# Kernel optimization log

Hardware: AMD Instinct MI355X
Metric: run time of the kernel (lower is better)

## Reference

```python
import jax, jax.numpy as jnp
import numpy as np


def gcn_conv(x, W, b, src, dst, edge_weight):
    """GCNConv: out = A_hat @ (x @ W) + b, with A_hat given as an edge list.
    x: [N, F_in], W: [F_in, F_out], src/dst: [E] int, edge_weight: [E]."""
    N = x.shape[0]
    support = x @ W                                   # [N, F_out] dense GEMM
    msgs = support[src] * edge_weight[:, None]        # [E, F_out] gather + scale
    agg = jax.ops.segment_sum(msgs, dst, num_segments=N)  # [N, F_out] scatter-add
    return agg + b


def setup_inputs() -> dict:
    key = jax.random.key(0)
    ks = jax.random.split(key, 8)
    N, E, F_IN, H, D = 100000, 1600000, 256, 128, 64
    feature = jax.random.normal(ks[0], (N, F_IN), dtype=jnp.float32)
    src = jax.random.randint(ks[1], (E,), 0, N)
    dst = jax.random.randint(ks[2], (E,), 0, N)
    edge_weight = jax.random.uniform(ks[3], (E,), dtype=jnp.float32)
    W1 = jax.random.normal(ks[4], (F_IN, H), dtype=jnp.float32) / np.sqrt(F_IN).astype(np.float32)
    b1 = jnp.zeros((H,), jnp.float32)
    W2 = jax.random.normal(ks[5], (H, D), dtype=jnp.float32) / np.sqrt(H).astype(np.float32)
    b2 = jnp.zeros((D,), jnp.float32)
    return {"feature": feature, "src": src, "dst": dst, "edge_weight": edge_weight,
            "W1": W1, "b1": b1, "W2": W2, "b2": b2}


def reference(feature, src, dst, edge_weight, W1, b1, W2, b2):
    # layer 1: GCNConv -> relu (dropout is identity in eval mode)
    x1 = jax.nn.relu(gcn_conv(feature, W1, b1, src, dst, edge_weight))
    # layer 2: GCNConv -> log_softmax over feature dim
    x2 = gcn_conv(x1, W2, b2, src, dst, edge_weight)
    return (x1, jax.nn.log_softmax(x2, axis=1))
```

## Files before the change

kernel.cpp:

```cpp
#include <hip/hip_runtime.h>
#include <hip/hip_bf16.h>
#include <type_traits>


typedef unsigned short u16;
typedef unsigned char  u8;

__device__ __forceinline__ u16 f2bf(float x) {
    union { float f; unsigned u; } v; v.f = x;
    const unsigned r = v.u + 0x7FFFu + ((v.u >> 16) & 1u);
    return (u16)(r >> 16);
}
__device__ __forceinline__ float bf2f(unsigned h) {
    union { unsigned u; float f; } v; v.u = h << 16;
    return v.f;
}
__device__ __forceinline__ float uaf(unsigned u) {
    union { unsigned u; float f; } v; v.u = u;
    return v.f;
}
__device__ __forceinline__ unsigned fau(float f) {
    union { float f; unsigned u; } v; v.f = f;
    return v.u;
}

using short8  = __attribute__((ext_vector_type(8))) short;
using float4v = __attribute__((ext_vector_type(4))) float;

#define TILE_A 8192

template <typename AT, int BNt>
__device__ __forceinline__ void gemm_body(
    const int bix, const AT* __restrict__ A, const u16* __restrict__ BT,
    u16* __restrict__ C, const int M, const int K)
{
    constexpr int BMt = 128;
    constexpr int WAVES_N = BNt / 64;
    constexpr int WROWS = 4 / WAVES_N;
    constexpr int WMF = BMt / (16 * WROWS);
    constexpr int WNF = 4;

    __shared__ __align__(16) u16 As[BMt * 32];
    __shared__ __align__(16) u16 Bs[BNt * 32];

    const int tid  = threadIdx.x;
    const int lane = tid & 63;
    const int w    = tid >> 6;
    const int m0   = bix * BMt;

    const int wm = (w % WROWS) * (WMF * 16);
    const int wn = (w / WROWS) * 64;

    const int fm = lane & 15;
    const int kh = lane >> 4;

    float4v acc[WMF][WNF] = {};

    for (int k0 = 0; k0 < K; k0 += 32) {
        __syncthreads();
        if constexpr (std::is_same<AT, float>::value) {
#pragma unroll
            for (int i = 0; i < 4; ++i) {
                const int s   = i * 256 + tid;
                const int row = s >> 3;
                const int seg = s & 7;
                const int gr  = min(m0 + row, M - 1);
                const float4 v = *(const float4*)&A[(size_t)gr * K + k0 + seg * 4];
                ushort4 o;
                o.x = f2bf(v.x); o.y = f2bf(v.y); o.z = f2bf(v.z); o.w = f2bf(v.w);
                *(ushort4*)&As[row * 32 + seg * 4] = o;
            }
        } else {
#pragma unroll
            for (int i = 0; i < 2; ++i) {
                const int s   = i * 256 + tid;
                const int row = s >> 2;
                const int seg = s & 3;
                const int gr  = min(m0 + row, M - 1);
                *(uint4*)&As[row * 32 + seg * 8] =
                    *(const uint4*)&A[(size_t)gr * K + k0 + seg * 8];
            }
        }
#pragma unroll
        for (int i = 0; i < BNt * 4 / 256; ++i) {
            const int s   = i * 256 + tid;
            const int row = s >> 2;
            const int seg = s & 3;
            *(uint4*)&Bs[row * 32 + seg * 8] =
                *(const uint4*)&BT[(size_t)row * K + k0 + seg * 8];
        }
        __syncthreads();

        short8 af[WMF], bfr[WNF];
#pragma unroll
        for (int i = 0; i < WMF; ++i)
            af[i] = *(const short8*)&As[(wm + i * 16 + fm) * 32 + kh * 8];
#pragma unroll
        for (int j = 0; j < WNF; ++j)
            bfr[j] = *(const short8*)&Bs[(wn + j * 16 + fm) * 32 + kh * 8];
#pragma unroll
        for (int i = 0; i < WMF; ++i)
#pragma unroll
            for (int j = 0; j < WNF; ++j)
                acc[i][j] = __builtin_amdgcn_mfma_f32_16x16x32_bf16(
                    af[i], bfr[j], acc[i][j], 0, 0, 0);
    }

#pragma unroll
    for (int i = 0; i < WMF; ++i) {
#pragma unroll
        for (int j = 0; j < WNF; ++j) {
            const int col = wn + j * 16 + fm;
#pragma unroll
            for (int r = 0; r < 4; ++r) {
                const int row = m0 + wm + i * 16 + kh * 4 + r;
                if (row < M) C[(size_t)row * BNt + col] = f2bf(acc[i][j][r]);
            }
        }
    }
}

__global__ __launch_bounds__(256) void gemm2_k(
    const float* __restrict__ A, const u16* __restrict__ BT,
    u16* __restrict__ C, int M, int K)
{
    gemm_body<float, 64>(blockIdx.x, A, BT, C, M, K);
}

__global__ __launch_bounds__(256) void sortA1_k(
    const int* __restrict__ dst, int* __restrict__ G, int E, int NBLK, int NB,
    const float* __restrict__ W1, u16* __restrict__ W1T, int K1, int N1,
    const float* __restrict__ W2, u16* __restrict__ W2T, int K2, int N2)
{
    const int b = blockIdx.x;
    if (b >= NBLK) {
        const int t = (b - NBLK) * 256 + threadIdx.x;
        const int tot1 = K1 * N1;
        if (t < tot1) {
            const int k = t % K1, nn = t / K1;
            W1T[(size_t)nn * K1 + k] = f2bf(W1[(size_t)k * N1 + nn]);
        } else {
            const int t2 = t - tot1;
            if (t2 < K2 * N2) {
                const int k = t2 % K2, nn = t2 / K2;
                W2T[(size_t)nn * K2 + k] = f2bf(W2[(size_t)k * N2 + nn]);
            }
        }
        return;
    }

    __shared__ int hist[512];
    for (int i = threadIdx.x; i < NB; i += 256) hist[i] = 0;
    __syncthreads();
    const int base = b * TILE_A;
#pragma unroll 4
    for (int i = 0; i < TILE_A; i += 256) {
        const int e = base + i + threadIdx.x;
        if (e < E) atomicAdd(&hist[((unsigned)dst[e]) >> 8], 1);
    }
    __syncthreads();
    for (int i = threadIdx.x; i < NB; i += 256)
        G[(size_t)i * NBLK + b] = hist[i];
}


#define SCAN_B 256
#define SCAN_I 8
#define SCAN_TILE (SCAN_B * SCAN_I)

__global__ __launch_bounds__(SCAN_B) void scan_pass1(
    const int* __restrict__ in, int* __restrict__ out,
    int* __restrict__ blockSums, int n)
{
    __shared__ int waveSums[SCAN_B / 64];
    const int tid = threadIdx.x;
    const int lane = tid & 63;
    const int wid = tid >> 6;
    const int base = blockIdx.x * SCAN_TILE + tid * SCAN_I;

    int items[SCAN_I];
    int tsum = 0;
#pragma unroll
    for (int i = 0; i < SCAN_I; ++i) {
        const int idx = base + i;
        items[i] = (idx < n) ? in[idx] : 0;
        tsum += items[i];
    }
    int x = tsum;
#pragma unroll
    for (int o = 1; o < 64; o <<= 1) {
        const int y = __shfl_up(x, o, 64);
        if (lane >= o) x += y;
    }
    if (lane == 63) waveSums[wid] = x;
    __syncthreads();
    if (tid == 0) {
        int acc = 0;
#pragma unroll
        for (int w = 0; w < SCAN_B / 64; ++w) {
            const int t = waveSums[w]; waveSums[w] = acc; acc += t;
        }
        blockSums[blockIdx.x] = acc;
    }
    __syncthreads();
    int texcl = x - tsum + waveSums[wid];
#pragma unroll
    for (int i = 0; i < SCAN_I; ++i) {
        const int idx = base + i;
        if (idx < n) out[idx] = texcl;
        texcl += items[i];
    }
}

__global__ void scan_pass2(int* __restrict__ blockSums, int nb)
{
    const int lane = threadIdx.x;
    int run = 0;
    for (int base = 0; base < nb; base += 64) {
        const int idx = base + lane;
        const int v = (idx < nb) ? blockSums[idx] : 0;
        int x = v;
#pragma unroll
        for (int o = 1; o < 64; o <<= 1) {
            const int y = __shfl_up(x, o, 64);
            if (lane >= o) x += y;
        }
        if (idx < nb) blockSums[idx] = run + x - v;
        run += __shfl(x, 63, 64);
    }
}

__global__ __launch_bounds__(SCAN_B) void scan3G_k(
    int* __restrict__ G, const int* __restrict__ blockSums, int n,
    int* __restrict__ offs, int N, int E)
{
    const int idx = blockIdx.x * blockDim.x + threadIdx.x;
    if (idx < n) G[idx] += blockSums[idx / SCAN_TILE];
    if (idx == 0) offs[N] = E;
}

__global__ __launch_bounds__(256) void sortA2_k(
    const int* __restrict__ src, const int* __restrict__ dst,
    const float* __restrict__ ew, const int* __restrict__ G,
    uint2* __restrict__ eps, u8* __restrict__ ldst, int E, int NBLK, int NB)
{
    const int b = blockIdx.x;
    __shared__ int cur[512];
    for (int i = threadIdx.x; i < NB; i += 256)
        cur[i] = G[(size_t)i * NBLK + b];
    __syncthreads();
    const int base = b * TILE_A;
#pragma unroll 4
    for (int i = 0; i < TILE_A; i += 256) {
        const int e = base + i + threadIdx.x;
        if (e < E) {
            const int d = dst[e];
            const int p = atomicAdd(&cur[((unsigned)d) >> 8], 1);
            eps[p]  = make_uint2((unsigned)src[e], fau(ew[e]));
            ldst[p] = (u8)(d & 255);
        }
    }
}

__global__ __launch_bounds__(256) void megaB_k(
    const uint2* __restrict__ eps, const u8* __restrict__ ldst,
    const int* __restrict__ G, int* __restrict__ offs,
    uint2* __restrict__ epack, int E, int NBLK, int NB, int N,
    const float* __restrict__ A, const u16* __restrict__ BT,
    u16* __restrict__ C, int M, int K, int GB)
{
    const int b = blockIdx.x;
    const int third = b / 3;
    int sort_id = -1, gemm_id = -1;
    if ((b % 3) == 0 && third < NB) sort_id = third;
    else gemm_id = b - min((b + 2) / 3, NB);

    if (gemm_id >= 0) {
        if (gemm_id < GB) gemm_body<float, 128>(gemm_id, A, BT, C, M, K);
        return;
    }

    const int tid = threadIdx.x;
    const int sb = sort_id;
    const int start = G[(size_t)sb * NBLK];
    const int endv  = (sb + 1 < NB) ? G[(size_t)(sb + 1) * NBLK] : E;

    __shared__ int h[256];
    __shared__ int wsum[4];
    h[tid] = 0;
    __syncthreads();
    for (int i = start + tid; i < endv; i += 256)
        atomicAdd(&h[ldst[i]], 1);
    __syncthreads();

    const int lane = tid & 63;
    const int w = tid >> 6;
    const int v = h[tid];
    int x = v;
#pragma unroll
    for (int o = 1; o < 64; o <<= 1) {
        const int y = __shfl_up(x, o, 64);
        if (lane >= o) x += y;
    }
    if (lane == 63) wsum[w] = x;
    __syncthreads();
    if (tid == 0) {
        int a = 0;
#pragma unroll
        for (int q = 0; q < 4; ++q) { const int t = wsum[q]; wsum[q] = a; a += t; }
    }
    __syncthreads();
    const int excl = start + (x - v) + wsum[w];

    const int node = sb * 256 + tid;
    if (node < N) offs[node] = excl;

    __syncthreads();
    h[tid] = excl;
    __syncthreads();

    for (int i = start + tid; i < endv; i += 256) {
        const uint2 ep = eps[i];
        const int p = atomicAdd(&h[ldst[i]], 1);
        epack[p] = ep;
    }
}


__global__ __launch_bounds__(256) void agg_f128b(
    const u16* __restrict__ sup, const int* __restrict__ offs,
    const uint2* __restrict__ epack, const float* __restrict__ bias,
    float* __restrict__ out, int N)
{
    const int node = (blockIdx.x * blockDim.x + threadIdx.x) >> 4;
    const int hl = threadIdx.x & 15;
    if (node >= N) return;

    const int beg = offs[node];
    const int end = offs[node + 1];

    float a[2][8] = {};
    for (int j = beg; j < end; j += 16) {
        uint2 e[16];
#pragma unroll
        for (int i = 0; i < 16; ++i) {
            const int jj = (j + i < end) ? (j + i) : (end - 1);
            e[i] = epack[jj];
        }
#pragma unroll
        for (int i = 0; i < 16; ++i)
            if (j + i >= end) e[i].y = 0u;
        uint4 v[16];
#pragma unroll
        for (int i = 0; i < 16; ++i)
            v[i] = *(const uint4*)&sup[(size_t)e[i].x * 128 + hl * 8];
#pragma unroll
        for (int i = 0; i < 16; ++i) {
            const float w = uaf(e[i].y);
            float* acc = a[i & 1];
            acc[0] = fmaf(bf2f(v[i].x & 0xffffu), w, acc[0]);
            acc[1] = fmaf(bf2f(v[i].x >> 16),     w, acc[1]);
            acc[2] = fmaf(bf2f(v[i].y & 0xffffu), w, acc[2]);
            acc[3] = fmaf(bf2f(v[i].y >> 16),     w, acc[3]);
            acc[4] = fmaf(bf2f(v[i].z & 0xffffu), w, acc[4]);
            acc[5] = fmaf(bf2f(v[i].z >> 16),     w, acc[5]);
            acc[6] = fmaf(bf2f(v[i].w & 0xffffu), w, acc[6]);
            acc[7] = fmaf(bf2f(v[i].w >> 16),     w, acc[7]);
        }
    }
    const float4 b0 = *(const float4*)&bias[hl * 8];
    const float4 b1 = *(const float4*)&bias[hl * 8 + 4];
    float4v o0, o1;
    o0[0] = fmaxf(a[0][0] + a[1][0] + b0.x, 0.f);
    o0[1] = fmaxf(a[0][1] + a[1][1] + b0.y, 0.f);
    o0[2] = fmaxf(a[0][2] + a[1][2] + b0.z, 0.f);
    o0[3] = fmaxf(a[0][3] + a[1][3] + b0.w, 0.f);
    o1[0] = fmaxf(a[0][4] + a[1][4] + b1.x, 0.f);
    o1[1] = fmaxf(a[0][5] + a[1][5] + b1.y, 0.f);
    o1[2] = fmaxf(a[0][6] + a[1][6] + b1.z, 0.f);
    o1[3] = fmaxf(a[0][7] + a[1][7] + b1.w, 0.f);
    float4v* orow = (float4v*)&out[(size_t)node * 128 + hl * 8];
    __builtin_nontemporal_store(o0, orow);
    __builtin_nontemporal_store(o1, orow + 1);
}

__global__ __launch_bounds__(256) void agg_f64_lsm(
    const u16* __restrict__ sup, const int* __restrict__ offs,
    const uint2* __restrict__ epack, const float* __restrict__ bias,
    float* __restrict__ out, int N)
{
    const int node = (blockIdx.x * blockDim.x + threadIdx.x) >> 4;
    const int hl = threadIdx.x & 15;
    if (node >= N) return;

    const int beg = offs[node];
    const int end = offs[node + 1];

    float a[2][4] = {};
    for (int j = beg; j < end; j += 16) {
        uint2 e[16];
#pragma unroll
        for (int i = 0; i < 16; ++i) {
            const int jj = (j + i < end) ? (j + i) : (end - 1);
            e[i] = epack[jj];
        }
#pragma unroll
        for (int i = 0; i < 16; ++i)
            if (j + i >= end) e[i].y = 0u;
        uint2 v[16];
#pragma unroll
        for (int i = 0; i < 16; ++i)
            v[i] = *(const uint2*)&sup[(size_t)e[i].x * 64 + hl * 4];
#pragma unroll
        for (int i = 0; i < 16; ++i) {
            const float w = uaf(e[i].y);
            float* acc = a[i & 1];
            acc[0] = fmaf(bf2f(v[i].x & 0xffffu), w, acc[0]);
            acc[1] = fmaf(bf2f(v[i].x >> 16),     w, acc[1]);
            acc[2] = fmaf(bf2f(v[i].y & 0xffffu), w, acc[2]);
            acc[3] = fmaf(bf2f(v[i].y >> 16),     w, acc[3]);
        }
    }

    const float4 b4 = *(const float4*)&bias[hl * 4];
    float z[4];
    z[0] = a[0][0] + a[1][0] + b4.x;
    z[1] = a[0][1] + a[1][1] + b4.y;
    z[2] = a[0][2] + a[1][2] + b4.z;
    z[3] = a[0][3] + a[1][3] + b4.w;

    float m = fmaxf(fmaxf(z[0], z[1]), fmaxf(z[2], z[3]));
#pragma unroll
    for (int o = 8; o > 0; o >>= 1) m = fmaxf(m, __shfl_xor(m, o, 64));
    float s = __expf(z[0] - m) + __expf(z[1] - m) + __expf(z[2] - m) + __expf(z[3] - m);
#pragma unroll
    for (int o = 8; o > 0; o >>= 1) s += __shfl_xor(s, o, 64);
    const float ls = __logf(s);
    float4v zo;
    zo[0] = z[0] - m - ls; zo[1] = z[1] - m - ls;
    zo[2] = z[2] - m - ls; zo[3] = z[3] - m - ls;
    __builtin_nontemporal_store(zo, (float4v*)&out[(size_t)node * 64 + hl * 4]);
}


extern "C" void kernel_launch(void* const* d_in, const int* in_sizes, int n_in,
                              void* d_out, int out_size, void* d_ws, size_t ws_size,
                              hipStream_t stream) {
    const float* feature = (const float*)d_in[0];
    const int*   src     = (const int*)d_in[1];
    const int*   dst     = (const int*)d_in[2];
    const float* ew      = (const float*)d_in[3];
    const float* W1      = (const float*)d_in[4];
    const float* b1      = (const float*)d_in[5];
    const float* W2      = (const float*)d_in[6];
    const float* b2      = (const float*)d_in[7];

    const int E    = in_sizes[1];
    const int H    = in_sizes[5];
    const int D    = in_sizes[7];
    const int F_IN = in_sizes[4] / H;
    const int N    = in_sizes[0] / F_IN;

    float* out_x1 = (float*)d_out;
    float* out_x2 = (float*)d_out + (size_t)N * H;

    const int NB   = (N + 255) >> 8;
    const int NBLK = (E + TILE_A - 1) / TILE_A;
    const int nG   = NB * NBLK;
    const int GB   = (N + 127) / 128;

    char* ws = (char*)d_ws;
    auto carve = [&](size_t bytes) {
        char* p = ws;
        ws += (bytes + 15) & ~(size_t)15;
        return p;
    };
    int*   G         = (int*)  carve((size_t)nG * sizeof(int));
    int*   blockSums = (int*)  carve(4096 * sizeof(int));
    int*   offs      = (int*)  carve((size_t)(N + 1) * sizeof(int));
    uint2* epack     = (uint2*)carve((size_t)E * sizeof(uint2));
    u16*   W1T       = (u16*)  carve((size_t)H * F_IN * sizeof(u16));
    u16*   W2T       = (u16*)  carve((size_t)D * H * sizeof(u16));
    u16*   supbf     = (u16*)  carve((size_t)N * H * sizeof(u16));
    u16*   scratch   = (u16*)  carve((size_t)N * H * sizeof(u16));
    uint2* eps  = (uint2*)scratch;
    u8*    ldst = (u8*)scratch + (size_t)E * sizeof(uint2);

    {
        const int TCB = (F_IN * H + H * D + 255) / 256;
        sortA1_k<<<NBLK + TCB, 256, 0, stream>>>(
            dst, G, E, NBLK, NB, W1, W1T, F_IN, H, W2, W2T, H, D);
    }

    const int nScanBlocks = (nG + SCAN_TILE - 1) / SCAN_TILE;
    scan_pass1<<<nScanBlocks, SCAN_B, 0, stream>>>(G, G, blockSums, nG);
    scan_pass2<<<1, 64, 0, stream>>>(blockSums, nScanBlocks);
    scan3G_k<<<(nG + SCAN_B - 1) / SCAN_B, SCAN_B, 0, stream>>>(
        G, blockSums, nG, offs, N, E);

    sortA2_k<<<NBLK, 256, 0, stream>>>(src, dst, ew, G, eps, ldst, E, NBLK, NB);

    {
        int grid = NB + GB;
        if (grid < 3 * NB - 2) grid = 3 * NB - 2;
        megaB_k<<<grid, 256, 0, stream>>>(
            eps, ldst, G, offs, epack, E, NBLK, NB, N,
            feature, W1T, supbf, N, F_IN, GB);
    }

    agg_f128b<<<(N * 16 + 255) / 256, 256, 0, stream>>>(
        supbf, offs, epack, b1, out_x1, N);

    gemm2_k<<<(N + 127) / 128, 256, 0, stream>>>(out_x1, W2T, supbf, N, H);
    agg_f64_lsm<<<(N * 16 + 255) / 256, 256, 0, stream>>>(
        supbf, offs, epack, b2, out_x2, N);
}
```

Baseline: 425.8 us.

## Stage per-block edge lists in LDS and widen threads per node to 32

Both aggregation kernels now cooperatively load the edge packs of 8 consecutive nodes into shared memory, up to 512 entries, and then read indices and weights from LDS. Edges beyond that cap fall back to global memory. Each node is now handled by 32 lanes with narrower per-lane feature loads (uint2 / 32-bit) instead of 16 lanes with uint4 / uint2. The goal is to cut redundant per-lane global edge loads and raise parallelism, at the cost of a block barrier, LDS use, narrower memory transactions, and, in agg_f128b, dropping the nontemporal stores.

```diff
diff --git a/kernel.cpp b/kernel.cpp
--- a/kernel.cpp
+++ b/kernel.cpp
@@ -327,61 +327,63 @@
 }
 
 
+#define AGG_CAP 512
+
 __global__ __launch_bounds__(256) void agg_f128b(
     const u16* __restrict__ sup, const int* __restrict__ offs,
     const uint2* __restrict__ epack, const float* __restrict__ bias,
     float* __restrict__ out, int N)
 {
-    const int node = (blockIdx.x * blockDim.x + threadIdx.x) >> 4;
-    const int hl = threadIdx.x & 15;
+    __shared__ uint2 se[AGG_CAP];
+    const int tid = threadIdx.x;
+    const int n0  = blockIdx.x * 8;
+    const int nE  = min(n0 + 8, N);
+    const int begB = offs[n0];
+    const int endB = offs[nE];
+    const int len  = endB - begB;
+    for (int i = tid; i < min(len, AGG_CAP); i += 256)
+        se[i] = epack[begB + i];
+    __syncthreads();
+
+    const int node = n0 + (tid >> 5);
+    const int hl   = tid & 31;
     if (node >= N) return;
 
     const int beg = offs[node];
     const int end = offs[node + 1];
 
-    float a[2][8] = {};
+    float a[2][4] = {};
     for (int j = beg; j < end; j += 16) {
-        uint2 e[16];
+        uint2 v[16];
 #pragma unroll
         for (int i = 0; i < 16; ++i) {
             const int jj = (j + i < end) ? (j + i) : (end - 1);
-            e[i] = epack[jj];
-        }
-#pragma unroll
-        for (int i = 0; i < 16; ++i)
-            if (j + i >= end) e[i].y = 0u;
-        uint4 v[16];
-#pragma unroll
-        for (int i = 0; i < 16; ++i)
-            v[i] = *(const uint4*)&sup[(size_t)e[i].x * 128 + hl * 8];
+            const int li = jj - begB;
+            const unsigned s = (li < AGG_CAP) ? se[li].x : epack[jj].x;
+            v[i] = *(const uint2*)&sup[(size_t)s * 128 + hl * 4];
+        }
 #pragma unroll
         for (int i = 0; i < 16; ++i) {
-            const float w = uaf(e[i].y);
+            const int jj = j + i;
+            float w = 0.f;
+            if (jj < end) {
+                const int li = jj - begB;
+                w = (li < AGG_CAP) ? uaf(se[li].y) : uaf(epack[jj].y);
+            }
             float* acc = a[i & 1];
             acc[0] = fmaf(bf2f(v[i].x & 0xffffu), w, acc[0]);
             acc[1] = fmaf(bf2f(v[i].x >> 16),     w, acc[1]);
             acc[2] = fmaf(bf2f(v[i].y & 0xffffu), w, acc[2]);
             acc[3] = fmaf(bf2f(v[i].y >> 16),     w, acc[3]);
-            acc[4] = fmaf(bf2f(v[i].z & 0xffffu), w, acc[4]);
-            acc[5] = fmaf(bf2f(v[i].z >> 16),     w, acc[5]);
-            acc[6] = fmaf(bf2f(v[i].w & 0xffffu), w, acc[6]);
-            acc[7] = fmaf(bf2f(v[i].w >> 16),     w, acc[7]);
-        }
-    }
-    const float4 b0 = *(const float4*)&bias[hl * 8];
-    const float4 b1 = *(const float4*)&bias[hl * 8 + 4];
-    float4v o0, o1;
-    o0[0] = fmaxf(a[0][0] + a[1][0] + b0.x, 0.f);
-    o0[1] = fmaxf(a[0][1] + a[1][1] + b0.y, 0.f);
-    o0[2] = fmaxf(a[0][2] + a[1][2] + b0.z, 0.f);
-    o0[3] = fmaxf(a[0][3] + a[1][3] + b0.w, 0.f);
-    o1[0] = fmaxf(a[0][4] + a[1][4] + b1.x, 0.f);
-    o1[1] = fmaxf(a[0][5] + a[1][5] + b1.y, 0.f);
-    o1[2] = fmaxf(a[0][6] + a[1][6] + b1.z, 0.f);
-    o1[3] = fmaxf(a[0][7] + a[1][7] + b1.w, 0.f);
-    float4v* orow = (float4v*)&out[(size_t)node * 128 + hl * 8];
-    __builtin_nontemporal_store(o0, orow);
-    __builtin_nontemporal_store(o1, orow + 1);
+        }
+    }
+    const float4 b4 = *(const float4*)&bias[hl * 4];
+    float4v o0;
+    o0[0] = fmaxf(a[0][0] + a[1][0] + b4.x, 0.f);
+    o0[1] = fmaxf(a[0][1] + a[1][1] + b4.y, 0.f);
+    o0[2] = fmaxf(a[0][2] + a[1][2] + b4.z, 0.f);
+    o0[3] = fmaxf(a[0][3] + a[1][3] + b4.w, 0.f);
+    *(float4v*)&out[(size_t)node * 128 + hl * 4] = o0;
 }
 
 __global__ __launch_bounds__(256) void agg_f64_lsm(
@@ -389,57 +391,64 @@
     const uint2* __restrict__ epack, const float* __restrict__ bias,
     float* __restrict__ out, int N)
 {
-    const int node = (blockIdx.x * blockDim.x + threadIdx.x) >> 4;
-    const int hl = threadIdx.x & 15;
+    __shared__ uint2 se[AGG_CAP];
+    const int tid = threadIdx.x;
+    const int n0  = blockIdx.x * 8;
+    const int nE  = min(n0 + 8, N);
+    const int begB = offs[n0];
+    const int endB = offs[nE];
+    const int len  = endB - begB;
+    for (int i = tid; i < min(len, AGG_CAP); i += 256)
+        se[i] = epack[begB + i];
+    __syncthreads();
+
+    const int node = n0 + (tid >> 5);
+    const int hl   = tid & 31;
     if (node >= N) return;
 
     const int beg = offs[node];
     const int end = offs[node + 1];
 
-    float a[2][4] = {};
+    float a[2][2] = {};
     for (int j = beg; j < end; j += 16) {
-        uint2 e[16];
+        unsigned v[16];
 #pragma unroll
         for (int i = 0; i < 16; ++i) {
             const int jj = (j + i < end) ? (j + i) : (end - 1);
-            e[i] = epack[jj];
-        }
-#pragma unroll
-        for (int i = 0; i < 16; ++i)
-            if (j + i >= end) e[i].y = 0u;
-        uint2 v[16];
-#pragma unroll
-        for (int i = 0; i < 16; ++i)
-            v[i] = *(const uint2*)&sup[(size_t)e[i].x * 64 + hl * 4];
+            const int li = jj - begB;
+            const unsigned s = (li < AGG_CAP) ? se[li].x : epack[jj].x;
+            v[i] = *(const unsigned*)&sup[(size_t)s * 64 + hl * 2];
+        }
 #pragma unroll
         for (int i = 0; i < 16; ++i) {
-            const float w = uaf(e[i].y);
+            const int jj = j + i;
+            float w = 0.f;
+            if (jj < end) {
+                const int li = jj - begB;
+                w = (li < AGG_CAP) ? uaf(se[li].y) : uaf(epack[jj].y);
+            }
             float* acc = a[i & 1];
-            acc[0] = fmaf(bf2f(v[i].x & 0xffffu), w, acc[0]);
-            acc[1] = fmaf(bf2f(v[i].x >> 16),     w, acc[1]);
-            acc[2] = fmaf(bf2f(v[i].y & 0xffffu), w, acc[2]);
-            acc[3] = fmaf(bf2f(v[i].y >> 16),     w, acc[3]);
-        }
-    }
-
-    const float4 b4 = *(const float4*)&bias[hl * 4];
-    float z[4];
-    z[0] = a[0][0] + a[1][0] + b4.x;
-    z[1] = a[0][1] + a[1][1] + b4.y;
-    z[2] = a[0][2] + a[1][2] + b4.z;
-    z[3] = a[0][3] + a[1][3] + b4.w;
-
-    float m = fmaxf(fmaxf(z[0], z[1]), fmaxf(z[2], z[3]));
-#pragma unroll
-    for (int o = 8; o > 0; o >>= 1) m = fmaxf(m, __shfl_xor(m, o, 64));
-    float s = __expf(z[0] - m) + __expf(z[1] - m) + __expf(z[2] - m) + __expf(z[3] - m);
-#pragma unroll
-    for (int o = 8; o > 0; o >>= 1) s += __shfl_xor(s, o, 64);
+            acc[0] = fmaf(bf2f(v[i] & 0xffffu), w, acc[0]);
+            acc[1] = fmaf(bf2f(v[i] >> 16),     w, acc[1]);
+        }
+    }
+
+    const float2 b2 = *(const float2*)&bias[hl * 2];
+    float z0 = a[0][0] + a[1][0] + b2.x;
+    float z1 = a[0][1] + a[1][1] + b2.y;
+
+    float m = fmaxf(z0, z1);
+#pragma unroll
+    for (int o = 16; o > 0; o >>= 1) m = fmaxf(m, __shfl_xor(m, o, 64));
+    float s = __expf(z0 - m) + __expf(z1 - m);
+#pragma unroll
+    for (int o = 16; o > 0; o >>= 1) s += __shfl_xor(s, o, 64);
     const float ls = __logf(s);
-    float4v zo;
-    zo[0] = z[0] - m - ls; zo[1] = z[1] - m - ls;
-    zo[2] = z[2] - m - ls; zo[3] = z[3] - m - ls;
-    __builtin_nontemporal_store(zo, (float4v*)&out[(size_t)node * 64 + hl * 4]);
+    using float2v = __attribute__((ext_vector_type(2))) float;
+    float2v zo;
+    zo[0] = z0 - m - ls;
+    zo[1] = z1 - m - ls;
+    __builtin_nontemporal_store(zo, (float2v*)&out[(size_t)node * 64 + hl * 2]);
 }
 
 
@@ -508,10 +517,10 @@
             feature, W1T, supbf, N, F_IN, GB);
     }
 
-    agg_f128b<<<(N * 16 + 255) / 256, 256, 0, stream>>>(
+    agg_f128b<<<(N + 7) / 8, 256, 0, stream>>>(
         supbf, offs, epack, b1, out_x1, N);
 
     gemm2_k<<<(N + 127) / 128, 256, 0, stream>>>(out_x1, W2T, supbf, N, H);
-    agg_f64_lsm<<<(N * 16 + 255) / 256, 256, 0, stream>>>(
+    agg_f64_lsm<<<(N + 7) / 8, 256, 0, stream>>>(
         supbf, offs, epack, b2, out_x2, N);
 }
```

New measurement: 432.4 us. About the same (+1.6%).
